# Kernel optimization log

Measured on AMD Instinct MI355X. Metric: run time of the kernel, lower is better.

## Reference

```python
import jax, jax.numpy as jnp
import numpy as np

B, N_HEADS, C_DIM, H_IMG, W_IMG = 4, 8, 256, 128, 128
N_TOK = H_IMG * W_IMG


def _ln(x, w, b, eps=1e-5):
    m = x.mean(-1, keepdims=True)
    v = ((x - m) ** 2).mean(-1, keepdims=True)
    return (x - m) * jax.lax.rsqrt(v + eps) * w + b


def _dwconv_pe(x, w, b, H, W):
    # x: [B, N, C]; depthwise 3x3 conv positional encoding with residual
    Bn, Nn, Cc = x.shape
    feat = x.transpose(0, 2, 1).reshape(Bn, Cc, H, W)
    feat = jax.lax.conv_general_dilated(
        feat, w, (1, 1), 'SAME', feature_group_count=Cc,
        dimension_numbers=('NCHW', 'OIHW', 'NCHW'))
    feat = feat + b[None, :, None, None]
    return x + feat.reshape(Bn, Cc, H * W).transpose(0, 2, 1)


def _xca(x, y, kv_w, q_w, proj_w, proj_b, h):
    # cross channel (covariance) attention: q from x, k/v from y
    Bn, Nn, Cc = x.shape
    hd = Cc // h
    scale = hd ** -0.5
    kv = (y @ kv_w).reshape(Bn, Nn, 2, h, hd)
    k = kv[:, :, 0].transpose(0, 2, 1, 3) * scale   # [B,h,N,hd]
    v = kv[:, :, 1].transpose(0, 2, 1, 3)           # [B,h,N,hd]
    q = (x @ q_w).reshape(Bn, Nn, h, hd).transpose(0, 2, 1, 3)
    attn = jax.nn.softmax(jnp.einsum('bhnd,bhne->bhde', k, v), axis=-1)  # [B,h,hd,hd]
    out = jnp.einsum('bhde,bhne->bhnd', attn, q)    # [B,h,N,hd]
    out = out.transpose(0, 2, 1, 3).reshape(Bn, Nn, Cc)
    return out @ proj_w + proj_b


def _forward(x, y, cpex0_w, cpex0_b, cpey0_w, cpey0_b, ln1x_w, ln1x_b, ln1y_w, ln1y_b,
             attnx_kv_w, attnx_q_w, attnx_proj_w, attnx_proj_b,
             attny_kv_w, attny_q_w, attny_proj_w, attny_proj_b,
             cpex1_w, cpex1_b, cpey1_w, cpey1_b,
             ci_w1, ci_b1, ci_w2, ci_b2, ln2_w, ln2_b,
             fc1_w, fc1_b, fc2_w, fc2_b, H, W):
    x = _dwconv_pe(x, cpex0_w, cpex0_b, H, W)
    y = _dwconv_pe(y, cpey0_w, cpey0_b, H, W)
    curx = _ln(x, ln1x_w, ln1x_b)
    cury = _ln(y, ln1y_w, ln1y_b)
    curx = _xca(curx, cury, attnx_kv_w, attnx_q_w, attnx_proj_w, attnx_proj_b, N_HEADS)
    cury = _xca(cury, curx, attny_kv_w, attny_q_w, attny_proj_w, attny_proj_b, N_HEADS)
    x = x + curx
    y = y + cury
    x = _dwconv_pe(x, cpex1_w, cpex1_b, H, W)
    y = _dwconv_pe(y, cpey1_w, cpey1_b, H, W)
    Bn, _, Cc = x.shape
    xi = x.transpose(0, 2, 1).reshape(Bn, Cc, H, W)
    yi = y.transpose(0, 2, 1).reshape(Bn, Cc, H, W)
    # SE-style channel interaction gating
    pooled = jnp.concatenate([xi.mean((2, 3)), yi.mean((2, 3))], axis=1)  # [B,2C]
    g = jax.nn.gelu(pooled @ ci_w1 + ci_b1, approximate=False)
    g = jax.nn.sigmoid(g @ ci_w2 + ci_b2)  # [B,2C]
    s_x = g[:, :Cc, None, None]
    s_y = g[:, Cc:, None, None]
    f = s_x * yi + s_y * xi  # [B,C,H,W]
    # MLP with residual
    ft = f.reshape(Bn, Cc, H * W).transpose(0, 2, 1)  # [B,N,C]
    hmid = _ln(ft, ln2_w, ln2_b)
    hmid = jax.nn.gelu(hmid @ fc1_w + fc1_b, approximate=False) @ fc2_w + fc2_b
    ft = ft + hmid
    return ft.transpose(0, 2, 1).reshape(Bn, Cc, H, W)


def setup_inputs() -> dict:
    key = jax.random.key(0)
    ks = iter(jax.random.split(key, 40))
    def rn(shape, s=0.02):
        return jax.random.normal(next(ks), shape, jnp.float32) * s
    C = C_DIM
    d = {}
    d['x'] = jax.random.normal(next(ks), (B, N_TOK, C), jnp.float32)
    d['y'] = jax.random.normal(next(ks), (B, N_TOK, C), jnp.float32)
    for nm in ['cpex0', 'cpey0', 'cpex1', 'cpey1']:
        d[nm + '_w'] = rn((C, 1, 3, 3))
        d[nm + '_b'] = jnp.zeros((C,), jnp.float32)
    for nm in ['ln1x', 'ln1y', 'ln2']:
        d[nm + '_w'] = jnp.ones((C,), jnp.float32)
        d[nm + '_b'] = jnp.zeros((C,), jnp.float32)
    for nm in ['attnx', 'attny']:
        d[nm + '_kv_w'] = rn((C, 2 * C))
        d[nm + '_q_w'] = rn((C, C))
        d[nm + '_proj_w'] = rn((C, C))
        d[nm + '_proj_b'] = jnp.zeros((C,), jnp.float32)
    d['ci_w1'] = rn((2 * C, C)); d['ci_b1'] = jnp.zeros((C,), jnp.float32)
    d['ci_w2'] = rn((C, 2 * C)); d['ci_b2'] = jnp.zeros((2 * C,), jnp.float32)
    d['fc1_w'] = rn((C, 4 * C)); d['fc1_b'] = jnp.zeros((4 * C,), jnp.float32)
    d['fc2_w'] = rn((4 * C, C)); d['fc2_b'] = jnp.zeros((C,), jnp.float32)
    d['H'] = H_IMG
    d['W'] = W_IMG
    return d


def reference(x, y, cpex0_w, cpex0_b, cpey0_w, cpey0_b, ln1x_w, ln1x_b, ln1y_w, ln1y_b,
              attnx_kv_w, attnx_q_w, attnx_proj_w, attnx_proj_b,
              attny_kv_w, attny_q_w, attny_proj_w, attny_proj_b,
              cpex1_w, cpex1_b, cpey1_w, cpey1_b,
              ci_w1, ci_b1, ci_w2, ci_b2, ln2_w, ln2_b,
              fc1_w, fc1_b, fc2_w, fc2_b, H, W):
    return _forward(x, y, cpex0_w, cpex0_b, cpey0_w, cpey0_b, ln1x_w, ln1x_b, ln1y_w, ln1y_b,
                    attnx_kv_w, attnx_q_w, attnx_proj_w, attnx_proj_b,
                    attny_kv_w, attny_q_w, attny_proj_w, attny_proj_b,
                    cpex1_w, cpex1_b, cpey1_w, cpey1_b,
                    ci_w1, ci_b1, ci_w2, ci_b2, ln2_w, ln2_b,
                    fc1_w, fc1_b, fc2_w, fc2_b, H, W)
```

## Files before the change

kernel.cpp:

```cpp
#include <hip/hip_runtime.h>
#include <hip/hip_bf16.h>

#define B_   4
#define C_   256
#define NTOK 16384
#define M_   (B_*NTOK)

typedef unsigned short u16;
typedef __attribute__((ext_vector_type(8))) short short8;
typedef __attribute__((ext_vector_type(4))) float f32x4;

#if defined(__has_builtin)
# if __has_builtin(__builtin_amdgcn_global_load_lds)
#  define HAVE_GLL 1
# endif
#endif
#ifndef HAVE_GLL
# define HAVE_GLL 0
#endif

__device__ __forceinline__ float gelu_exact(float x) {
    return 0.5f * x * (1.f + erff(x * 0.70710678118654752f));
}
__device__ __forceinline__ u16 f2bf(float f) {
    __hip_bfloat16 h = __float2bfloat16(f);
    return *reinterpret_cast<u16*>(&h);
}

#if HAVE_GLL
__device__ __forceinline__ void gload16(const void* g, void* lds_uniform) {
    __builtin_amdgcn_global_load_lds((const __attribute__((address_space(1))) unsigned int*)g,
                                     (__attribute__((address_space(3))) unsigned int*)lds_uniform,
                                     16, 0, 0);
}
#endif

template<bool LN_A, bool HAS_BIAS, int ACT, bool HAS_RES, bool OUT_F32, bool OUT_BF16, bool ATOMIC>
__launch_bounds__(256)
__global__ void gemm_mfma(const u16* __restrict__ Abf, const float* __restrict__ Af,
                          const float2* __restrict__ stats, const float* __restrict__ lnw,
                          const float* __restrict__ lnb,
                          const u16* __restrict__ Bt, const float* __restrict__ bias,
                          const float* __restrict__ res, float* __restrict__ outf,
                          u16* __restrict__ outb,
                          int K, int ldA, int ldB, int N, int nsplit,
                          size_t aBS, size_t bBS, size_t oBS, size_t rBS) {
    __shared__ __align__(16) u16 As[128 * 64];
    __shared__ __align__(16) u16 Bs[128 * 64];
    const int tid = threadIdx.x;
    const int bm = blockIdx.y * 128, bn = blockIdx.x * 128;
    int batch = blockIdx.z, split = 0;
    if (nsplit > 1) { batch = blockIdx.z / nsplit; split = blockIdx.z - batch * nsplit; }
    const int KL = K / nsplit;
    const int kb = split * KL;
    const size_t aoff = (size_t)batch * aBS, boff = (size_t)batch * bBS;
    const size_t ooff = (size_t)batch * oBS, roff = (size_t)batch * rBS;
    const size_t soff = (size_t)batch * NTOK;

    const int lane = tid & 63, wv = tid >> 6;
    const int wm = wv >> 1, wn = wv & 1;
    const int r16 = lane & 15, kg = lane >> 4;

    f32x4 acc[4][4];
#pragma unroll
    for (int i = 0; i < 4; i++)
#pragma unroll
        for (int j = 0; j < 4; j++) acc[i][j] = (f32x4){0.f, 0.f, 0.f, 0.f};

    for (int kk = 0; kk < KL; kk += 64) {
        const int k0 = kb + kk;
#pragma unroll
        for (int it = 0; it < 4; it++) {
            const int chunk = it * 256 + tid;
            const int row = chunk >> 3, c = chunk & 7;
            const int g = c ^ (row & 7);
            const u16* gp = Bt + boff + (size_t)(bn + row) * ldB + k0 + g * 8;
#if HAVE_GLL
            gload16(gp, (char*)Bs + it * 4096 + wv * 1024);
#else
            *(uint4*)((char*)Bs + chunk * 16) = *(const uint4*)gp;
#endif
        }
        if constexpr (LN_A) {
#pragma unroll
            for (int q = 0; q < 4; q++) {
                const int chunk = q * 256 + tid;
                const int row = chunk >> 3, c = chunk & 7;
                const int g = c ^ (row & 7);
                const float* ap = Af + aoff + (size_t)(bm + row) * ldA + k0 + c * 8;
                const float2 st = stats[soff + bm + row];
                const float4 v0 = *(const float4*)ap;
                const float4 v1 = *(const float4*)(ap + 4);
                const float* w = lnw + k0 + c * 8;
                const float* bb = lnb + k0 + c * 8;
                u16 u[8];
                u[0] = f2bf((v0.x - st.x) * st.y * w[0] + bb[0]);
                u[1] = f2bf((v0.y - st.x) * st.y * w[1] + bb[1]);
                u[2] = f2bf((v0.z - st.x) * st.y * w[2] + bb[2]);
                u[3] = f2bf((v0.w - st.x) * st.y * w[3] + bb[3]);
                u[4] = f2bf((v1.x - st.x) * st.y * w[4] + bb[4]);
                u[5] = f2bf((v1.y - st.x) * st.y * w[5] + bb[5]);
                u[6] = f2bf((v1.z - st.x) * st.y * w[6] + bb[6]);
                u[7] = f2bf((v1.w - st.x) * st.y * w[7] + bb[7]);
                uint4 pk;
                pk.x = (unsigned)u[0] | ((unsigned)u[1] << 16);
                pk.y = (unsigned)u[2] | ((unsigned)u[3] << 16);
                pk.z = (unsigned)u[4] | ((unsigned)u[5] << 16);
                pk.w = (unsigned)u[6] | ((unsigned)u[7] << 16);
                *(uint4*)&As[row * 64 + g * 8] = pk;
            }
        } else {
#pragma unroll
            for (int it = 0; it < 4; it++) {
                const int chunk = it * 256 + tid;
                const int row = chunk >> 3, c = chunk & 7;
                const int g = c ^ (row & 7);
                const u16* gp = Abf + aoff + (size_t)(bm + row) * ldA + k0 + g * 8;
#if HAVE_GLL
                gload16(gp, (char*)As + it * 4096 + wv * 1024);
#else
                *(uint4*)((char*)As + chunk * 16) = *(const uint4*)gp;
#endif
            }
        }
        __syncthreads();
        short8 af[4][2], bfr[4][2];
#pragma unroll
        for (int t = 0; t < 4; t++) {
#pragma unroll
            for (int kh = 0; kh < 2; kh++) {
                const int lc = kh * 4 + kg;
                const int ra = wm * 64 + t * 16 + r16;
                const int rb = wn * 64 + t * 16 + r16;
                af[t][kh]  = *(const short8*)&As[ra * 64 + ((lc ^ (ra & 7)) << 3)];
                bfr[t][kh] = *(const short8*)&Bs[rb * 64 + ((lc ^ (rb & 7)) << 3)];
            }
        }
#pragma unroll
        for (int mt = 0; mt < 4; mt++)
#pragma unroll
            for (int nt = 0; nt < 4; nt++)
#pragma unroll
                for (int kh = 0; kh < 2; kh++)
                    acc[mt][nt] = __builtin_amdgcn_mfma_f32_16x16x32_bf16(
                        af[mt][kh], bfr[nt][kh], acc[mt][nt], 0, 0, 0);
        __syncthreads();
    }
#pragma unroll
    for (int mt = 0; mt < 4; mt++) {
        const int gm0 = bm + wm * 64 + mt * 16 + kg * 4;
#pragma unroll
        for (int nt = 0; nt < 4; nt++) {
            const int gn = bn + wn * 64 + nt * 16 + r16;
            float bv = 0.f;
            if constexpr (HAS_BIAS) bv = bias[gn];
#pragma unroll
            for (int r = 0; r < 4; r++) {
                float v = acc[mt][nt][r];
                const size_t oi = (size_t)(gm0 + r) * N + gn;
                if constexpr (ATOMIC) {
                    atomicAdd(&outf[ooff + oi], v);
                } else {
                    v += bv;
                    if constexpr (ACT == 1) v = gelu_exact(v);
                    if constexpr (OUT_BF16) outb[ooff + oi] = f2bf(v);
                    if constexpr (HAS_RES) v += res[roff + oi];
                    if constexpr (OUT_F32) outf[ooff + oi] = v;
                }
            }
        }
    }
}

template<bool DO_STATS, bool DO_POOL>
__launch_bounds__(256)
__global__ void dwconv_pe_kernel(const float* __restrict__ in, const float* __restrict__ wconv,
                                 const float* __restrict__ bconv, float* __restrict__ out,
                                 float2* __restrict__ stats, float* __restrict__ pooled,
                                 int pool_off) {
    const int b = blockIdx.y;
    const int n0 = blockIdx.x * 16;
    const int h = n0 >> 7;
    const int w0 = n0 & 127;
    const int c = threadIdx.x;
    float wr[9];
#pragma unroll
    for (int i = 0; i < 9; i++) wr[i] = wconv[c * 9 + i];
    const float bb = bconv[c];
    const float* base = in  + (size_t)b * NTOK * C_ + c;
    float* obase      = out + (size_t)b * NTOK * C_ + c;
    float pacc = 0.f;
    __shared__ float red[8];
    const int lane = c & 63, wv = c >> 6;
    for (int t = 0; t < 16; t++) {
        const int w = w0 + t;
        float val = bb;
#pragma unroll
        for (int dh = -1; dh <= 1; dh++) {
            const int h2 = h + dh;
            if ((unsigned)h2 < 128u) {
#pragma unroll
                for (int dw = -1; dw <= 1; dw++) {
                    const int w2 = w + dw;
                    if ((unsigned)w2 < 128u)
                        val += wr[(dh + 1) * 3 + (dw + 1)] * base[((size_t)(h2 << 7) + w2) * C_];
                }
            }
        }
        const size_t oidx = ((size_t)(h << 7) + w) * C_;
        const float o = base[oidx] + val;
        obase[oidx] = o;
        if constexpr (DO_POOL) pacc += o;
        if constexpr (DO_STATS) {
            float sx = o, sy = o * o;
#pragma unroll
            for (int off = 32; off; off >>= 1) { sx += __shfl_xor(sx, off); sy += __shfl_xor(sy, off); }
            if (lane == 0) { red[wv * 2] = sx; red[wv * 2 + 1] = sy; }
            __syncthreads();
            const float tsx = red[0] + red[2] + red[4] + red[6];
            const float tsy = red[1] + red[3] + red[5] + red[7];
            __syncthreads();
            if (c == 0) {
                const float mean = tsx * (1.f / 256.f);
                const float var  = tsy * (1.f / 256.f) - mean * mean;
                stats[(size_t)b * NTOK + n0 + t] = make_float2(mean, rsqrtf(var + 1e-5f));
            }
        }
    }
    if constexpr (DO_POOL) atomicAdd(&pooled[b * 512 + pool_off + c], pacc);
}

template<bool LN>
__launch_bounds__(256)
__global__ void tbf16_kernel(const float* __restrict__ inF, const u16* __restrict__ inB,
                             const float2* __restrict__ stats, const float* __restrict__ lnw,
                             const float* __restrict__ lnb, u16* __restrict__ outT) {
    const int b = blockIdx.z;
    const int tok0 = blockIdx.x * 64, c0 = blockIdx.y * 64;
    const int tid = threadIdx.x;
    __shared__ __align__(16) u16 tile[64][72];
    if constexpr (LN) {
        const float* ib = inF + (size_t)b * NTOK * C_;
#pragma unroll
        for (int q = 0; q < 4; q++) {
            const int chunk = q * 256 + tid;
            const int row = chunk >> 4, c4 = (chunk & 15) * 4;
            const float2 st = stats[(size_t)b * NTOK + tok0 + row];
            const float4 v = *(const float4*)&ib[(size_t)(tok0 + row) * C_ + c0 + c4];
            tile[c4 + 0][row] = f2bf((v.x - st.x) * st.y * lnw[c0 + c4 + 0] + lnb[c0 + c4 + 0]);
            tile[c4 + 1][row] = f2bf((v.y - st.x) * st.y * lnw[c0 + c4 + 1] + lnb[c0 + c4 + 1]);
            tile[c4 + 2][row] = f2bf((v.z - st.x) * st.y * lnw[c0 + c4 + 2] + lnb[c0 + c4 + 2]);
            tile[c4 + 3][row] = f2bf((v.w - st.x) * st.y * lnw[c0 + c4 + 3] + lnb[c0 + c4 + 3]);
        }
    } else {
        const u16* ib = inB + (size_t)b * NTOK * C_;
#pragma unroll
        for (int q = 0; q < 2; q++) {
            const int chunk = q * 256 + tid;
            const int row = chunk >> 3, c8 = (chunk & 7) * 8;
            const uint4 u = *(const uint4*)&ib[(size_t)(tok0 + row) * C_ + c0 + c8];
            tile[c8 + 0][row] = (u16)(u.x & 0xffffu); tile[c8 + 1][row] = (u16)(u.x >> 16);
            tile[c8 + 2][row] = (u16)(u.y & 0xffffu); tile[c8 + 3][row] = (u16)(u.y >> 16);
            tile[c8 + 4][row] = (u16)(u.z & 0xffffu); tile[c8 + 5][row] = (u16)(u.z >> 16);
            tile[c8 + 6][row] = (u16)(u.w & 0xffffu); tile[c8 + 7][row] = (u16)(u.w >> 16);
        }
    }
    __syncthreads();
    const int cr = tid >> 2, tch = (tid & 3) * 16;
    u16* op = outT + (size_t)b * C_ * NTOK + (size_t)(c0 + cr) * NTOK + tok0 + tch;
    *(uint4*)op       = *(const uint4*)&tile[cr][tch];
    *(uint4*)(op + 8) = *(const uint4*)&tile[cr][tch + 8];
}

__launch_bounds__(256)
__global__ void wtrans_kernel(const float* __restrict__ in, u16* __restrict__ out, int K, int N) {
    const int n0 = blockIdx.x * 32, k0 = blockIdx.y * 32;
    const int tid = threadIdx.x;
    __shared__ float t[32][33];
#pragma unroll
    for (int q = 0; q < 4; q++) {
        const int chunk = q * 256 + tid;
        const int r = chunk >> 5, c = chunk & 31;
        t[r][c] = in[(size_t)(k0 + r) * N + n0 + c];
    }
    __syncthreads();
#pragma unroll
    for (int q = 0; q < 4; q++) {
        const int chunk = q * 256 + tid;
        const int r = chunk >> 5, c = chunk & 31;
        out[(size_t)(n0 + r) * K + k0 + c] = f2bf(t[c][r]);
    }
}

__launch_bounds__(256)
__global__ void sfromg_kernel(const float* __restrict__ G, const float* __restrict__ kv_w,
                              float* __restrict__ SM) {
    const int b = blockIdx.x >> 3, hh = blockIdx.x & 7;
    const int tid = threadIdx.x;
    __shared__ float Tl[256][33];
    __shared__ float Wvl[32][33];
    float acc[32];
#pragma unroll
    for (int e = 0; e < 32; e++) acc[e] = 0.f;
    const float* Gb = G + (size_t)b * 65536;
    for (int c0 = 0; c0 < 256; c0 += 32) {
#pragma unroll
        for (int q = 0; q < 8; q++) {
            const int idx = q * 256 + tid;
            const int r = idx >> 3, c4 = (idx & 7) * 4;
            *(float4*)&Tl[r][c4] = *(const float4*)&Gb[(size_t)r * 256 + c0 + c4];
        }
        {
            const int cc = tid >> 3, e4 = (tid & 7) * 4;
            *(float4*)&Wvl[cc][e4] = *(const float4*)&kv_w[(size_t)(c0 + cc) * 512 + 256 + hh * 32 + e4];
        }
        __syncthreads();
#pragma unroll 4
        for (int cc = 0; cc < 32; cc++) {
            const float g = Tl[tid][cc];
#pragma unroll
            for (int e = 0; e < 32; e++) acc[e] += g * Wvl[cc][e];
        }
        __syncthreads();
    }
#pragma unroll
    for (int e = 0; e < 32; e++) Tl[tid][e] = acc[e];
    __syncthreads();
    const int e = tid & 31, d0 = (tid >> 5) * 4;
    float s[4] = {0.f, 0.f, 0.f, 0.f};
    for (int r = 0; r < 256; r++) {
        const float t = Tl[r][e];
#pragma unroll
        for (int i = 0; i < 4; i++) s[i] += kv_w[(size_t)r * 512 + hh * 32 + d0 + i] * t;
    }
#pragma unroll
    for (int i = 0; i < 4; i++)
        SM[((size_t)(b * 8 + hh) * 32 + d0 + i) * 32 + e] = s[i] * 0.17677669529663687f;
}

__launch_bounds__(256)
__global__ void softmax32_kernel(float* __restrict__ Sm) {
    const int row = blockIdx.x * 8 + (threadIdx.x >> 5);
    const int e = threadIdx.x & 31;
    float v = Sm[row * 32 + e];
    float m = v;
#pragma unroll
    for (int off = 16; off; off >>= 1) m = fmaxf(m, __shfl_xor(m, off, 32));
    const float ex = expf(v - m);
    float s = ex;
#pragma unroll
    for (int off = 16; off; off >>= 1) s += __shfl_xor(s, off, 32);
    Sm[row * 32 + e] = ex / s;
}

__launch_bounds__(256)
__global__ void weff1_kernel(const float* __restrict__ q_w, const float* __restrict__ SM,
                             float* __restrict__ T1) {
    const int b = blockIdx.x >> 3, hh = blockIdx.x & 7;
    const int tid = threadIdx.x;
    __shared__ float A[32][33];
    {
        const int d = tid >> 3, e4 = (tid & 7) * 4;
        *(float4*)&A[d][e4] = *(const float4*)&SM[((size_t)(b * 8 + hh) * 32 + d) * 32 + e4];
    }
    __syncthreads();
    float qr[32];
#pragma unroll
    for (int e4 = 0; e4 < 8; e4++)
        *(float4*)&qr[e4 * 4] = *(const float4*)&q_w[(size_t)tid * 256 + hh * 32 + e4 * 4];
    float o[32];
#pragma unroll 4
    for (int d = 0; d < 32; d++) {
        float s = 0.f;
#pragma unroll
        for (int e = 0; e < 32; e++) s += qr[e] * A[d][e];
        o[d] = s;
    }
#pragma unroll
    for (int d4 = 0; d4 < 8; d4++)
        *(float4*)&T1[(size_t)b * 65536 + (size_t)tid * 256 + hh * 32 + d4 * 4] = *(float4*)&o[d4 * 4];
}

__launch_bounds__(256)
__global__ void weff2_kernel(const float* __restrict__ T1, const float* __restrict__ pw,
                             u16* __restrict__ WTb) {
    const int b = blockIdx.z;
    const int i0 = blockIdx.y * 64, j0 = blockIdx.x * 64;
    __shared__ float As2[16][64];
    __shared__ float Bs2[16][64];
    const int tid = threadIdx.x;
    const int tx = tid & 15, ty = tid >> 4;
    float acc[4][4];
#pragma unroll
    for (int i = 0; i < 4; i++)
#pragma unroll
        for (int j = 0; j < 4; j++) acc[i][j] = 0.f;
    const int ar = tid >> 2, ak4 = (tid & 3) * 4;
    const int bk = tid >> 4, bj4 = (tid & 15) * 4;
    for (int k0 = 0; k0 < 256; k0 += 16) {
        float4 av = *(const float4*)&T1[(size_t)b * 65536 + (size_t)(i0 + ar) * 256 + k0 + ak4];
        As2[ak4 + 0][ar] = av.x; As2[ak4 + 1][ar] = av.y;
        As2[ak4 + 2][ar] = av.z; As2[ak4 + 3][ar] = av.w;
        *(float4*)&Bs2[bk][bj4] = *(const float4*)&pw[(size_t)(k0 + bk) * 256 + j0 + bj4];
        __syncthreads();
#pragma unroll
        for (int kk = 0; kk < 16; kk++) {
            float a[4], c4[4];
            *(float4*)&a[0]  = *(const float4*)&As2[kk][ty * 4];
            *(float4*)&c4[0] = *(const float4*)&Bs2[kk][tx * 4];
#pragma unroll
            for (int i = 0; i < 4; i++)
#pragma unroll
                for (int j = 0; j < 4; j++) acc[i][j] += a[i] * c4[j];
        }
        __syncthreads();
    }
#pragma unroll
    for (int i = 0; i < 4; i++)
#pragma unroll
        for (int j = 0; j < 4; j++)
            WTb[(size_t)b * 65536 + (size_t)(j0 + tx * 4 + j) * 256 + i0 + ty * 4 + i] =
                f2bf(acc[i][j]);
}

__launch_bounds__(256)
__global__ void ci_kernel(const float* __restrict__ pooled, const float* __restrict__ w1,
                          const float* __restrict__ b1, const float* __restrict__ w2,
                          const float* __restrict__ b2, float* __restrict__ g) {
    const int b = blockIdx.x, t = threadIdx.x;
    __shared__ float pl[512];
    __shared__ float hid[256];
    pl[t]       = pooled[b * 512 + t]       * (1.f / NTOK);
    pl[t + 256] = pooled[b * 512 + 256 + t] * (1.f / NTOK);
    __syncthreads();
    float h = b1[t];
    for (int k = 0; k < 512; k++) h += pl[k] * w1[k * 256 + t];
    hid[t] = gelu_exact(h);
    __syncthreads();
    float g0 = b2[t], g1 = b2[t + 256];
    for (int k = 0; k < 256; k++) {
        const float hv = hid[k];
        g0 += hv * w2[k * 512 + t];
        g1 += hv * w2[k * 512 + 256 + t];
    }
    g[b * 512 + t]       = 1.f / (1.f + expf(-g0));
    g[b * 512 + 256 + t] = 1.f / (1.f + expf(-g1));
}

__launch_bounds__(256)
__global__ void fcomb_kernel(const float* __restrict__ g, const float* __restrict__ x2,
                             const float* __restrict__ y2, const float* __restrict__ lnw,
                             const float* __restrict__ lnb, float* __restrict__ ft,
                             u16* __restrict__ ftl) {
    const int b = blockIdx.y;
    const int n0 = blockIdx.x * 16;
    const int c = threadIdx.x;
    const float sx = g[b * 512 + c];
    const float sy = g[b * 512 + 256 + c];
    const float lw = lnw[c], lb = lnb[c];
    const size_t base = ((size_t)b * NTOK + n0) * C_ + c;
    __shared__ float red[8];
    const int lane = c & 63, wv = c >> 6;
    for (int t = 0; t < 16; t++) {
        const size_t idx = base + (size_t)t * C_;
        const float f = sx * y2[idx] + sy * x2[idx];
        ft[idx] = f;
        float vx = f, vy = f * f;
#pragma unroll
        for (int off = 32; off; off >>= 1) { vx += __shfl_xor(vx, off); vy += __shfl_xor(vy, off); }
        if (lane == 0) { red[wv * 2] = vx; red[wv * 2 + 1] = vy; }
        __syncthreads();
        const float tsx = red[0] + red[2] + red[4] + red[6];
        const float tsy = red[1] + red[3] + red[5] + red[7];
        __syncthreads();
        const float mean = tsx * (1.f / 256.f);
        const float var  = tsy * (1.f / 256.f) - mean * mean;
        ftl[idx] = f2bf((f - mean) * rsqrtf(var + 1e-5f) * lw + lb);
    }
}

__launch_bounds__(256)
__global__ void transpose_kernel(const float* __restrict__ in, float* __restrict__ out) {
    __shared__ float tile[32][33];
    const int b = blockIdx.z;
    const int n0 = blockIdx.x * 32, c0 = blockIdx.y * 32;
    const int tx = threadIdx.x & 31, ty = threadIdx.x >> 5;
    const float* ip = in + (size_t)b * NTOK * C_;
#pragma unroll
    for (int i = 0; i < 32; i += 8)
        tile[ty + i][tx] = ip[(size_t)(n0 + ty + i) * C_ + c0 + tx];
    __syncthreads();
    float* op = out + (size_t)b * C_ * NTOK;
#pragma unroll
    for (int i = 0; i < 32; i += 8)
        op[(size_t)(c0 + ty + i) * NTOK + n0 + tx] = tile[tx][ty + i];
}

extern "C" void kernel_launch(void* const* d_in, const int* in_sizes, int n_in,
                              void* d_out, int out_size, void* d_ws, size_t ws_size,
                              hipStream_t stream) {
    const float* x        = (const float*)d_in[0];
    const float* y        = (const float*)d_in[1];
    const float* cpex0_w  = (const float*)d_in[2];
    const float* cpex0_b  = (const float*)d_in[3];
    const float* cpey0_w  = (const float*)d_in[4];
    const float* cpey0_b  = (const float*)d_in[5];
    const float* cpex1_w  = (const float*)d_in[6];
    const float* cpex1_b  = (const float*)d_in[7];
    const float* cpey1_w  = (const float*)d_in[8];
    const float* cpey1_b  = (const float*)d_in[9];
    const float* ln1x_w   = (const float*)d_in[10];
    const float* ln1x_b   = (const float*)d_in[11];
    const float* ln1y_w   = (const float*)d_in[12];
    const float* ln1y_b   = (const float*)d_in[13];
    const float* ln2_w    = (const float*)d_in[14];
    const float* ln2_b    = (const float*)d_in[15];
    const float* attnx_kv = (const float*)d_in[16];
    const float* attnx_q  = (const float*)d_in[17];
    const float* attnx_pw = (const float*)d_in[18];
    const float* attnx_pb = (const float*)d_in[19];
    const float* attny_kv = (const float*)d_in[20];
    const float* attny_q  = (const float*)d_in[21];
    const float* attny_pw = (const float*)d_in[22];
    const float* attny_pb = (const float*)d_in[23];
    const float* ci_w1    = (const float*)d_in[24];
    const float* ci_b1    = (const float*)d_in[25];
    const float* ci_w2    = (const float*)d_in[26];
    const float* ci_b2    = (const float*)d_in[27];
    const float* fc1_b    = (const float*)d_in[29];
    const float* fc1_w    = (const float*)d_in[28];
    const float* fc2_w    = (const float*)d_in[30];
    const float* fc2_b    = (const float*)d_in[31];
    (void)in_sizes; (void)n_in; (void)out_size; (void)ws_size;

    const size_t S = (size_t)M_ * C_;
    float* ws = (float*)d_ws;
    float2* STX   = (float2*)(ws + 0);
    float2* STY   = (float2*)(ws + 131072);
    float*  GRAM  = ws + 262144;
    float*  SM    = ws + 524288;
    float*  T1    = ws + 557056;
    u16*    WTB   = (u16*)(ws + 819200);
    u16*    FC1WT = (u16*)(ws + 950272);
    u16*    FC2WT = (u16*)(ws + 1081344);
    float*  PL    = ws + 1212416;
    float*  GT    = ws + 1214464;
    float*  W0  = ws + 2097152;
    float*  W1  = W0 + S;
    float*  W2  = W1 + S;
    u16*    W2a = (u16*)W2;
    u16*    W2b = (u16*)(W2 + S / 2);
    float*  OUT = (float*)d_out;
    u16*    HID = (u16*)d_out;

    const dim3 blk(256);
    const dim3 g_dw(NTOK / 16, B_);
    const dim3 g_tb(NTOK / 64, C_ / 64, B_);
    const size_t SB = 4194304;

    wtrans_kernel<<<dim3(32, 8), blk, 0, stream>>>(fc1_w, FC1WT, 256, 1024);
    wtrans_kernel<<<dim3(8, 32), blk, 0, stream>>>(fc2_w, FC2WT, 1024, 256);

    dwconv_pe_kernel<true, false><<<g_dw, blk, 0, stream>>>(x, cpex0_w, cpex0_b, W0, STX, nullptr, 0);
    dwconv_pe_kernel<true, false><<<g_dw, blk, 0, stream>>>(y, cpey0_w, cpey0_b, W1, STY, nullptr, 0);

    tbf16_kernel<true><<<g_tb, blk, 0, stream>>>(W1, nullptr, STY, ln1y_w, ln1y_b, W2a);
    hipMemsetAsync(GRAM, 0, 262144 * sizeof(float), stream);
    gemm_mfma<false, false, 0, false, false, false, true><<<dim3(2, 2, 64), blk, 0, stream>>>(
        W2a, nullptr, nullptr, nullptr, nullptr, W2a, nullptr, nullptr, GRAM, nullptr,
        NTOK, NTOK, NTOK, 256, 16, SB, SB, 65536, 0);
    sfromg_kernel<<<dim3(32), blk, 0, stream>>>(GRAM, attnx_kv, SM);
    softmax32_kernel<<<dim3(128), blk, 0, stream>>>(SM);
    weff1_kernel<<<dim3(32), blk, 0, stream>>>(attnx_q, SM, T1);
    weff2_kernel<<<dim3(4, 4, B_), blk, 0, stream>>>(T1, attnx_pw, WTB);
    gemm_mfma<true, true, 0, true, true, true, false><<<dim3(2, 128, B_), blk, 0, stream>>>(
        nullptr, W0, STX, ln1x_w, ln1x_b, WTB, attnx_pb, W0, W0, W2b,
        256, 256, 256, 256, 1, SB, 65536, SB, SB);

    tbf16_kernel<false><<<g_tb, blk, 0, stream>>>(nullptr, W2b, nullptr, nullptr, nullptr, W2a);
    hipMemsetAsync(GRAM, 0, 262144 * sizeof(float), stream);
    gemm_mfma<false, false, 0, false, false, false, true><<<dim3(2, 2, 64), blk, 0, stream>>>(
        W2a, nullptr, nullptr, nullptr, nullptr, W2a, nullptr, nullptr, GRAM, nullptr,
        NTOK, NTOK, NTOK, 256, 16, SB, SB, 65536, 0);
    sfromg_kernel<<<dim3(32), blk, 0, stream>>>(GRAM, attny_kv, SM);
    softmax32_kernel<<<dim3(128), blk, 0, stream>>>(SM);
    weff1_kernel<<<dim3(32), blk, 0, stream>>>(attny_q, SM, T1);
    weff2_kernel<<<dim3(4, 4, B_), blk, 0, stream>>>(T1, attny_pw, WTB);
    gemm_mfma<true, true, 0, true, true, false, false><<<dim3(2, 128, B_), blk, 0, stream>>>(
        nullptr, W1, STY, ln1y_w, ln1y_b, WTB, attny_pb, W1, W1, nullptr,
        256, 256, 256, 256, 1, SB, 65536, SB, SB);

    hipMemsetAsync(PL, 0, 2048 * sizeof(float), stream);
    dwconv_pe_kernel<false, true><<<g_dw, blk, 0, stream>>>(W0, cpex1_w, cpex1_b, OUT, nullptr, PL, 0);
    dwconv_pe_kernel<false, true><<<g_dw, blk, 0, stream>>>(W1, cpey1_w, cpey1_b, W0, nullptr, PL, 256);

    ci_kernel<<<dim3(B_), blk, 0, stream>>>(PL, ci_w1, ci_b1, ci_w2, ci_b2, GT);
    fcomb_kernel<<<g_dw, blk, 0, stream>>>(GT, OUT, W0, ln2_w, ln2_b, W1, W2a);

    for (int h = 0; h < 2; h++) {
        gemm_mfma<false, true, 1, false, false, true, false><<<dim3(4, 512, 1), blk, 0, stream>>>(
            W2a, nullptr, nullptr, nullptr, nullptr, FC1WT + h * 512 * 256, fc1_b + h * 512,
            nullptr, nullptr, HID, 256, 256, 256, 512, 1, 0, 0, 0, 0);
        if (h == 0)
            gemm_mfma<false, true, 0, true, true, false, false><<<dim3(2, 512, 1), blk, 0, stream>>>(
                HID, nullptr, nullptr, nullptr, nullptr, FC2WT, fc2_b, W1, W1, nullptr,
                512, 512, 1024, 256, 1, 0, 0, 0, 0);
        else
            gemm_mfma<false, false, 0, true, true, false, false><<<dim3(2, 512, 1), blk, 0, stream>>>(
                HID, nullptr, nullptr, nullptr, nullptr, FC2WT + 512, nullptr, W1, W1, nullptr,
                512, 512, 1024, 256, 1, 0, 0, 0, 0);
    }

    transpose_kernel<<<dim3(NTOK / 32, C_ / 32, B_), blk, 0, stream>>>(W1, OUT);
}
```

Before: 1.415 ms.

## Rewrite depthwise conv as sliding-window row kernel and vectorize fcomb

The depthwise 3x3 conv becomes a row-strip kernel. Each wave owns 4 image rows and 4 channels per lane, and slides a column window along width so each input column is loaded once and reused, with float4 loads and stores. LayerNorm stats are reduced within a wave via shuffles instead of block-level shared-memory syncs. fcomb is likewise vectorized to float4 with one wave per token and packed bf16 stores. The conv grid shrinks to 8x4 blocks, so only a few waves run per device, which risks severe underutilization and low memory bandwidth for a memory-bound op.

```diff
diff --git a/kernel.cpp b/kernel.cpp
--- a/kernel.cpp
+++ b/kernel.cpp
@@ -174,60 +174,88 @@
 
 template<bool DO_STATS, bool DO_POOL>
 __launch_bounds__(256)
-__global__ void dwconv_pe_kernel(const float* __restrict__ in, const float* __restrict__ wconv,
-                                 const float* __restrict__ bconv, float* __restrict__ out,
-                                 float2* __restrict__ stats, float* __restrict__ pooled,
-                                 int pool_off) {
+__global__ void dwconv_row_kernel(const float* __restrict__ in, const float* __restrict__ wconv,
+                                  const float* __restrict__ bconv, float* __restrict__ out,
+                                  float2* __restrict__ stats, float* __restrict__ pooled,
+                                  int pool_off) {
     const int b = blockIdx.y;
-    const int n0 = blockIdx.x * 16;
-    const int h = n0 >> 7;
-    const int w0 = n0 & 127;
-    const int c = threadIdx.x;
-    float wr[9];
-#pragma unroll
-    for (int i = 0; i < 9; i++) wr[i] = wconv[c * 9 + i];
-    const float bb = bconv[c];
-    const float* base = in  + (size_t)b * NTOK * C_ + c;
-    float* obase      = out + (size_t)b * NTOK * C_ + c;
-    float pacc = 0.f;
-    __shared__ float red[8];
-    const int lane = c & 63, wv = c >> 6;
-    for (int t = 0; t < 16; t++) {
-        const int w = w0 + t;
-        float val = bb;
-#pragma unroll
-        for (int dh = -1; dh <= 1; dh++) {
-            const int h2 = h + dh;
-            if ((unsigned)h2 < 128u) {
-#pragma unroll
-                for (int dw = -1; dw <= 1; dw++) {
-                    const int w2 = w + dw;
-                    if ((unsigned)w2 < 128u)
-                        val += wr[(dh + 1) * 3 + (dw + 1)] * base[((size_t)(h2 << 7) + w2) * C_];
-                }
-            }
-        }
-        const size_t oidx = ((size_t)(h << 7) + w) * C_;
-        const float o = base[oidx] + val;
-        obase[oidx] = o;
-        if constexpr (DO_POOL) pacc += o;
+    const int tid = threadIdx.x;
+    const int wv = tid >> 6, lane = tid & 63;
+    const int r0 = blockIdx.x * 16 + wv * 4;
+    const int c4 = lane * 4;
+
+    float4 wr[9];
+#pragma unroll
+    for (int t = 0; t < 9; t++)
+        wr[t] = make_float4(wconv[(c4 + 0) * 9 + t], wconv[(c4 + 1) * 9 + t],
+                            wconv[(c4 + 2) * 9 + t], wconv[(c4 + 3) * 9 + t]);
+    const float4 bb = *(const float4*)&bconv[c4];
+
+    const float* ibase = in  + (size_t)b * NTOK * C_ + c4;
+    float* obase       = out + (size_t)b * NTOK * C_ + c4;
+    const float4 z4 = make_float4(0.f, 0.f, 0.f, 0.f);
+    float4 colP[6], colC[6], colN[6];
+    bool rv[6];
+#pragma unroll
+    for (int j = 0; j < 6; j++) {
+        const int gr = r0 - 1 + j;
+        rv[j] = (unsigned)gr < 128u;
+        colP[j] = z4;
+        colC[j] = rv[j] ? *(const float4*)&ibase[((size_t)(gr << 7) + 0) * C_] : z4;
+        colN[j] = rv[j] ? *(const float4*)&ibase[((size_t)(gr << 7) + 1) * C_] : z4;
+    }
+    float4 pacc = z4;
+
+    for (int w = 0; w < 128; w++) {
+        float4 nxt[6];
+        const bool wok = (w + 2) < 128;
+#pragma unroll
+        for (int j = 0; j < 6; j++)
+            nxt[j] = (wok && rv[j]) ? *(const float4*)&ibase[((size_t)((r0 - 1 + j) << 7) + w + 2) * C_] : z4;
+
+        float s[4], q[4];
+#pragma unroll
+        for (int i = 0; i < 4; i++) {
+            float4 v = bb;
+#pragma unroll
+            for (int dh = 0; dh < 3; dh++) {
+                const float4 p = colP[i + dh], c = colC[i + dh], n = colN[i + dh];
+                const float4 w0 = wr[dh * 3 + 0], w1 = wr[dh * 3 + 1], w2 = wr[dh * 3 + 2];
+                v.x += w0.x * p.x + w1.x * c.x + w2.x * n.x;
+                v.y += w0.y * p.y + w1.y * c.y + w2.y * n.y;
+                v.z += w0.z * p.z + w1.z * c.z + w2.z * n.z;
+                v.w += w0.w * p.w + w1.w * c.w + w2.w * n.w;
+            }
+            const float4 ctr = colC[i + 1];
+            float4 o = make_float4(ctr.x + v.x, ctr.y + v.y, ctr.z + v.z, ctr.w + v.w);
+            *(float4*)&obase[((size_t)((r0 + i) << 7) + w) * C_] = o;
+            if constexpr (DO_POOL) { pacc.x += o.x; pacc.y += o.y; pacc.z += o.z; pacc.w += o.w; }
+            if constexpr (DO_STATS) {
+                s[i] = o.x + o.y + o.z + o.w;
+                q[i] = o.x * o.x + o.y * o.y + o.z * o.z + o.w * o.w;
+            }
+        }
         if constexpr (DO_STATS) {
-            float sx = o, sy = o * o;
-#pragma unroll
-            for (int off = 32; off; off >>= 1) { sx += __shfl_xor(sx, off); sy += __shfl_xor(sy, off); }
-            if (lane == 0) { red[wv * 2] = sx; red[wv * 2 + 1] = sy; }
-            __syncthreads();
-            const float tsx = red[0] + red[2] + red[4] + red[6];
-            const float tsy = red[1] + red[3] + red[5] + red[7];
-            __syncthreads();
-            if (c == 0) {
-                const float mean = tsx * (1.f / 256.f);
-                const float var  = tsy * (1.f / 256.f) - mean * mean;
-                stats[(size_t)b * NTOK + n0 + t] = make_float2(mean, rsqrtf(var + 1e-5f));
-            }
-        }
-    }
-    if constexpr (DO_POOL) atomicAdd(&pooled[b * 512 + pool_off + c], pacc);
+#pragma unroll
+            for (int off = 32; off; off >>= 1) {
+#pragma unroll
+                for (int i = 0; i < 4; i++) { s[i] += __shfl_xor(s[i], off); q[i] += __shfl_xor(q[i], off); }
+            }
+            if (lane < 4) {
+                const float mean = s[lane] * (1.f / 256.f);
+                const float var  = q[lane] * (1.f / 256.f) - mean * mean;
+                stats[(size_t)b * NTOK + ((r0 + lane) << 7) + w] = make_float2(mean, rsqrtf(var + 1e-5f));
+            }
+        }
+#pragma unroll
+        for (int j = 0; j < 6; j++) { colP[j] = colC[j]; colC[j] = colN[j]; colN[j] = nxt[j]; }
+    }
+    if constexpr (DO_POOL) {
+        atomicAdd(&pooled[b * 512 + pool_off + c4 + 0], pacc.x);
+        atomicAdd(&pooled[b * 512 + pool_off + c4 + 1], pacc.y);
+        atomicAdd(&pooled[b * 512 + pool_off + c4 + 2], pacc.z);
+        atomicAdd(&pooled[b * 512 + pool_off + c4 + 3], pacc.w);
+    }
 }
 
 template<bool LN>
@@ -453,29 +481,36 @@
                              const float* __restrict__ lnb, float* __restrict__ ft,
                              u16* __restrict__ ftl) {
     const int b = blockIdx.y;
-    const int n0 = blockIdx.x * 16;
-    const int c = threadIdx.x;
-    const float sx = g[b * 512 + c];
-    const float sy = g[b * 512 + 256 + c];
-    const float lw = lnw[c], lb = lnb[c];
-    const size_t base = ((size_t)b * NTOK + n0) * C_ + c;
-    __shared__ float red[8];
-    const int lane = c & 63, wv = c >> 6;
-    for (int t = 0; t < 16; t++) {
-        const size_t idx = base + (size_t)t * C_;
-        const float f = sx * y2[idx] + sy * x2[idx];
-        ft[idx] = f;
-        float vx = f, vy = f * f;
-#pragma unroll
-        for (int off = 32; off; off >>= 1) { vx += __shfl_xor(vx, off); vy += __shfl_xor(vy, off); }
-        if (lane == 0) { red[wv * 2] = vx; red[wv * 2 + 1] = vy; }
-        __syncthreads();
-        const float tsx = red[0] + red[2] + red[4] + red[6];
-        const float tsy = red[1] + red[3] + red[5] + red[7];
-        __syncthreads();
-        const float mean = tsx * (1.f / 256.f);
-        const float var  = tsy * (1.f / 256.f) - mean * mean;
-        ftl[idx] = f2bf((f - mean) * rsqrtf(var + 1e-5f) * lw + lb);
+    const int tid = threadIdx.x;
+    const int wv = tid >> 6, lane = tid & 63;
+    const int n0 = blockIdx.x * 256 + wv * 64;
+    const int c4 = lane * 4;
+    const float4 sx = *(const float4*)&g[b * 512 + c4];
+    const float4 sy = *(const float4*)&g[b * 512 + 256 + c4];
+    const float4 lw = *(const float4*)&lnw[c4];
+    const float4 lb = *(const float4*)&lnb[c4];
+    for (int t = 0; t < 64; t++) {
+        const size_t idx = ((size_t)b * NTOK + n0 + t) * C_ + c4;
+        const float4 xv = *(const float4*)&x2[idx];
+        const float4 yv = *(const float4*)&y2[idx];
+        float4 f;
+        f.x = sx.x * yv.x + sy.x * xv.x;
+        f.y = sx.y * yv.y + sy.y * xv.y;
+        f.z = sx.z * yv.z + sy.z * xv.z;
+        f.w = sx.w * yv.w + sy.w * xv.w;
+        *(float4*)&ft[idx] = f;
+        float s = f.x + f.y + f.z + f.w;
+        float q = f.x * f.x + f.y * f.y + f.z * f.z + f.w * f.w;
+#pragma unroll
+        for (int off = 32; off; off >>= 1) { s += __shfl_xor(s, off); q += __shfl_xor(q, off); }
+        const float mean = s * (1.f / 256.f);
+        const float rstd = rsqrtf(q * (1.f / 256.f) - mean * mean + 1e-5f);
+        uint2 pk;
+        pk.x = (unsigned)f2bf((f.x - mean) * rstd * lw.x + lb.x)
+             | ((unsigned)f2bf((f.y - mean) * rstd * lw.y + lb.y) << 16);
+        pk.y = (unsigned)f2bf((f.z - mean) * rstd * lw.z + lb.z)
+             | ((unsigned)f2bf((f.w - mean) * rstd * lw.w + lb.w) << 16);
+        *(uint2*)&ftl[idx] = pk;
     }
 }
 
@@ -527,8 +562,8 @@
     const float* ci_b1    = (const float*)d_in[25];
     const float* ci_w2    = (const float*)d_in[26];
     const float* ci_b2    = (const float*)d_in[27];
+    const float* fc1_w    = (const float*)d_in[28];
     const float* fc1_b    = (const float*)d_in[29];
-    const float* fc1_w    = (const float*)d_in[28];
     const float* fc2_w    = (const float*)d_in[30];
     const float* fc2_b    = (const float*)d_in[31];
     (void)in_sizes; (void)n_in; (void)out_size; (void)ws_size;
@@ -554,15 +589,16 @@
     u16*    HID = (u16*)d_out;
 
     const dim3 blk(256);
-    const dim3 g_dw(NTOK / 16, B_);
+    const dim3 g_dw(8, B_);
+    const dim3 g_fc(NTOK / 256, B_);
     const dim3 g_tb(NTOK / 64, C_ / 64, B_);
     const size_t SB = 4194304;
 
     wtrans_kernel<<<dim3(32, 8), blk, 0, stream>>>(fc1_w, FC1WT, 256, 1024);
     wtrans_kernel<<<dim3(8, 32), blk, 0, stream>>>(fc2_w, FC2WT, 1024, 256);
 
-    dwconv_pe_kernel<true, false><<<g_dw, blk, 0, stream>>>(x, cpex0_w, cpex0_b, W0, STX, nullptr, 0);
-    dwconv_pe_kernel<true, false><<<g_dw, blk, 0, stream>>>(y, cpey0_w, cpey0_b, W1, STY, nullptr, 0);
+    dwconv_row_kernel<true, false><<<g_dw, blk, 0, stream>>>(x, cpex0_w, cpex0_b, W0, STX, nullptr, 0);
+    dwconv_row_kernel<true, false><<<g_dw, blk, 0, stream>>>(y, cpey0_w, cpey0_b, W1, STY, nullptr, 0);
 
     tbf16_kernel<true><<<g_tb, blk, 0, stream>>>(W1, nullptr, STY, ln1y_w, ln1y_b, W2a);
     hipMemsetAsync(GRAM, 0, 262144 * sizeof(float), stream);
@@ -591,11 +627,11 @@
         256, 256, 256, 256, 1, SB, 65536, SB, SB);
 
     hipMemsetAsync(PL, 0, 2048 * sizeof(float), stream);
-    dwconv_pe_kernel<false, true><<<g_dw, blk, 0, stream>>>(W0, cpex1_w, cpex1_b, OUT, nullptr, PL, 0);
-    dwconv_pe_kernel<false, true><<<g_dw, blk, 0, stream>>>(W1, cpey1_w, cpey1_b, W0, nullptr, PL, 256);
+    dwconv_row_kernel<false, true><<<g_dw, blk, 0, stream>>>(W0, cpex1_w, cpex1_b, OUT, nullptr, PL, 0);
+    dwconv_row_kernel<false, true><<<g_dw, blk, 0, stream>>>(W1, cpey1_w, cpey1_b, W0, nullptr, PL, 256);
 
     ci_kernel<<<dim3(B_), blk, 0, stream>>>(PL, ci_w1, ci_b1, ci_w2, ci_b2, GT);
-    fcomb_kernel<<<g_dw, blk, 0, stream>>>(GT, OUT, W0, ln2_w, ln2_b, W1, W2a);
+    fcomb_kernel<<<g_fc, blk, 0, stream>>>(GT, OUT, W0, ln2_w, ln2_b, W1, W2a);
 
     for (int h = 0; h < 2; h++) {
         gemm_mfma<false, true, 1, false, false, true, false><<<dim3(4, 512, 1), blk, 0, stream>>>(
```

Measured after the change: 1.682 ms. +18.9%, slower.
